# Kernel tuning notes

Hardware: AMD Instinct MI355X
Metric: run time of the kernel (lower is better)

## Reference

```python
import jax, jax.numpy as jnp
import numpy as np

N, F, RBF, E = 25000, 64, 32, 400000
RC = 5.0  # maximum_interaction_radius


def _tensor_norm(t):
    # Frobenius norm squared over the trailing 3x3 dims
    return (t ** 2).sum((-2, -1))


def _decompose(t):
    # X = I + A + S (irreducible decomposition of 3x3 blocks)
    diag_mean = jnp.trace(t, axis1=-2, axis2=-1) / 3.0
    I = diag_mean[..., None, None] * jnp.eye(3, dtype=t.dtype)
    A = 0.5 * (t - jnp.swapaxes(t, -2, -1))
    S = 0.5 * (t + jnp.swapaxes(t, -2, -1)) - I
    return I, A, S


def _lin(t, W):
    # feature-dim linear (no bias) on [N, F, 3, 3]
    return jnp.einsum('nfij,gf->ngij', t, W)


def setup_inputs():
    key = jax.random.key(0)
    ks = jax.random.split(key, 17)
    f32 = jnp.float32
    return {
        'X': jax.random.normal(ks[0], (N, F, 3, 3), f32),
        'pair_indices': jax.random.randint(ks[1], (2, E), 0, N),
        'd_ij': jax.random.uniform(ks[2], (E, 1), f32) * RC,
        'radial_feature_vector': jax.random.normal(ks[3], (E, RBF), f32),
        'atomic_charges': jax.random.normal(ks[4], (N,), f32) * 0.1,
        'W1': jax.random.normal(ks[5], (F, RBF), f32) / np.sqrt(RBF),
        'b1': jnp.zeros((F,), f32),
        'W2': jax.random.normal(ks[6], (2 * F, F), f32) / np.sqrt(F),
        'b2': jnp.zeros((2 * F,), f32),
        'W3': jax.random.normal(ks[7], (3 * F, 2 * F), f32) / np.sqrt(2 * F),
        'b3': jnp.zeros((3 * F,), f32),
        'Wl0': jax.random.normal(ks[8], (F, F), f32) / np.sqrt(F),
        'Wl1': jax.random.normal(ks[9], (F, F), f32) / np.sqrt(F),
        'Wl2': jax.random.normal(ks[10], (F, F), f32) / np.sqrt(F),
        'Wl3': jax.random.normal(ks[11], (F, F), f32) / np.sqrt(F),
        'Wl4': jax.random.normal(ks[12], (F, F), f32) / np.sqrt(F),
        'Wl5': jax.random.normal(ks[13], (F, F), f32) / np.sqrt(F),
    }


def reference(X, pair_indices, d_ij, radial_feature_vector, atomic_charges,
              W1, b1, W2, b2, W3, b3, Wl0, Wl1, Wl2, Wl3, Wl4, Wl5):
    act = jax.nn.silu
    # cosine attenuation cutoff
    C = jnp.where(d_ij < RC, 0.5 * (jnp.cos(jnp.pi * d_ij / RC) + 1.0), 0.0).reshape(-1, 1)
    # mlp_scalar: rbf -> F -> 2F -> 3F, SiLU after each Dense
    h = act(radial_feature_vector @ W1.T + b1)
    h = act(h @ W2.T + b2)
    h = act(h @ W3.T + b3) * C
    rfv = h.reshape(-1, F, 3)  # [E, F, 3]

    Xn = X / (_tensor_norm(X) + 1.0)[..., None, None]
    I, A, S = _decompose(Xn)
    I = _lin(I, Wl0)
    A = _lin(A, Wl1)
    S = _lin(S, Wl2)
    Y = I + A + S

    src, dst = pair_indices[0], pair_indices[1]

    def mp(comp, t):
        # gather-scale-scatter: [E,F,1,1] * gather([N,F,3,3]) -> scatter-add
        msg = comp[:, :, None, None] * t[dst]
        return jax.ops.segment_sum(msg, src, num_segments=N)

    msg = mp(rfv[..., 0], I) + mp(rfv[..., 1], A) + mp(rfv[..., 2], S)

    # O(3) branch
    MA = jnp.matmul(msg, Y)
    MB = jnp.matmul(Y, msg)
    scale = 1.0 + 0.1 * atomic_charges[:, None, None, None]
    I, A, S = _decompose(scale * (MA + MB))
    normp1 = (_tensor_norm(I + A + S) + 1.0)[..., None, None]
    I, A, S = I / normp1, A / normp1, S / normp1
    I = _lin(I, Wl3)
    A = _lin(A, Wl4)
    S = _lin(S, Wl5)
    dX = I + A + S
    return Xn + dX + scale * jnp.matmul(dX, dX)
```

## Files before the change

### kernel.cpp

```cpp
#include <hip/hip_runtime.h>
#include <hip/hip_fp16.h>
#include <math.h>

#ifndef M_PI
#define M_PI 3.14159265358979323846
#endif


typedef _Float16 f16x8 __attribute__((ext_vector_type(8)));
typedef float f32x4 __attribute__((ext_vector_type(4)));

#define AROW 216
#define MLPFRAGS 34816
#define WLFRAG 4096

__device__ __forceinline__ float silu_f(float x) {
    return x / (1.0f + __expf(-x));
}

__device__ __forceinline__ void recon(const float u[9], float M[9]) {
    M[0] =  u[0] + u[4];
    M[1] =  u[1] + u[5];
    M[2] =  u[2] + u[6];
    M[3] = -u[1] + u[5];
    M[4] =  u[0] + u[7];
    M[5] =  u[3] + u[8];
    M[6] = -u[2] + u[6];
    M[7] = -u[3] + u[8];
    M[8] =  u[0] - u[4] - u[7];
}

__global__ __launch_bounds__(256) void k_wcvt(
    const float* __restrict__ W1, const float* __restrict__ W2,
    const float* __restrict__ W3,
    const float* __restrict__ Wl0, const float* __restrict__ Wl1,
    const float* __restrict__ Wl2, const float* __restrict__ Wl3,
    const float* __restrict__ Wl4, const float* __restrict__ Wl5,
    __half* __restrict__ Wf)
{
    int idx = blockIdx.x * 256 + threadIdx.x;
    if (idx >= MLPFRAGS + 6 * WLFRAG) return;
    float v;
    if (idx < MLPFRAGS) {
        int frag = idx >> 9;
        int r = idx & 511;
        int l = r >> 3, j = r & 7;
        int l15 = l & 15, lg = l >> 4;
        if (frag < 4) {
            int ct = frag;
            v = W1[(ct * 16 + l15) * 32 + (lg * 8 + j)];
        } else if (frag < 20) {
            int f2 = frag - 4;
            int ct = f2 >> 1, ks = f2 & 1;
            v = W2[(ct * 16 + l15) * 64 + (ks * 32 + lg * 8 + j)];
        } else {
            int f3 = frag - 20;
            int ct = f3 >> 2, ks = f3 & 3;
            v = W3[(ct * 16 + l15) * 128 + (ks * 32 + lg * 8 + j)];
        }
    } else {
        int r2 = idx - MLPFRAGS;
        int wIdx = r2 >> 12;
        int rr = r2 & 4095;
        int f = rr >> 9;
        int ct = f >> 1, ks = f & 1;
        int elem = rr & 511;
        int l = elem >> 3, j = elem & 7;
        int l15 = l & 15, lg = l >> 4;
        const float* W = (wIdx == 0) ? Wl0 : (wIdx == 1) ? Wl1 : (wIdx == 2) ? Wl2
                       : (wIdx == 3) ? Wl3 : (wIdx == 4) ? Wl4 : Wl5;
        v = W[(ct * 16 + l15) * 64 + (ks * 32 + lg * 8 + j)];
    }
    Wf[idx] = __float2half(v);
}

__global__ __launch_bounds__(256) void k_head(
    const float* __restrict__ X, const __half* __restrict__ Wfrag,
    __half2* __restrict__ TgP, uint2* __restrict__ Tg456, int N)
{
    __shared__ __half u2l[9 * 32 * 72];
    __shared__ float s_x[2304];
    int tid = threadIdx.x;
    int n0 = blockIdx.x * 32;
    size_t total = (size_t)N * 576;

    for (int ch = 0; ch < 8; ++ch) {
        size_t base = (size_t)(n0 + ch * 4) * 576;
        for (int idx = tid; idx < 2304; idx += 256) {
            size_t gi = base + idx;
            s_x[idx] = (gi < total) ? X[gi] : 0.f;
        }
        __syncthreads();
        int w = tid >> 6, f = tid & 63;
        int node = ch * 4 + w;
        float m[9]; float n2 = 0.f;
#pragma unroll
        for (int i = 0; i < 9; ++i) { m[i] = s_x[w * 576 + f * 9 + i]; n2 += m[i] * m[i]; }
        float inv = 1.0f / (n2 + 1.0f);
#pragma unroll
        for (int i = 0; i < 9; ++i) m[i] *= inv;
        float lam = (m[0] + m[4] + m[8]) * (1.f / 3.f);
        u2l[(0 * 32 + node) * 72 + f] = __float2half(lam);
        u2l[(1 * 32 + node) * 72 + f] = __float2half(0.5f * (m[1] - m[3]));
        u2l[(2 * 32 + node) * 72 + f] = __float2half(0.5f * (m[2] - m[6]));
        u2l[(3 * 32 + node) * 72 + f] = __float2half(0.5f * (m[5] - m[7]));
        u2l[(4 * 32 + node) * 72 + f] = __float2half(m[0] - lam);
        u2l[(5 * 32 + node) * 72 + f] = __float2half(0.5f * (m[1] + m[3]));
        u2l[(6 * 32 + node) * 72 + f] = __float2half(0.5f * (m[2] + m[6]));
        u2l[(7 * 32 + node) * 72 + f] = __float2half(m[4] - lam);
        u2l[(8 * 32 + node) * 72 + f] = __float2half(0.5f * (m[5] + m[7]));
        __syncthreads();
    }

    int w = tid >> 6, lane = tid & 63;
    int l15 = lane & 15, lg = lane >> 4;
    const f32x4 z = {0.f, 0.f, 0.f, 0.f};
    f32x4 acc[5][4];
#pragma unroll
    for (int q = 0; q < 5; ++q) {
        int cm = w + q * 4;
        if (cm < 18) {
            int c = cm >> 1, rt = cm & 1;
            int gsel = (c == 0) ? 0 : (c < 4 ? 1 : 2);
            const f16x8* WFc = (const f16x8*)(Wfrag + gsel * WLFRAG);
            int abase = (c * 32 + rt * 16 + l15) * 72;
            f16x8 a0 = *(const f16x8*)&u2l[abase + lg * 8];
            f16x8 a1 = *(const f16x8*)&u2l[abase + 32 + lg * 8];
#pragma unroll
            for (int ct = 0; ct < 4; ++ct) {
                acc[q][ct] = __builtin_amdgcn_mfma_f32_16x16x32_f16(a0, WFc[(ct * 2 + 0) * 64 + lane], z, 0, 0, 0);
                acc[q][ct] = __builtin_amdgcn_mfma_f32_16x16x32_f16(a1, WFc[(ct * 2 + 1) * 64 + lane], acc[q][ct], 0, 0, 0);
            }
        }
    }
    __syncthreads();
#pragma unroll
    for (int q = 0; q < 5; ++q) {
        int cm = w + q * 4;
        if (cm < 18) {
            int c = cm >> 1, rt = cm & 1;
#pragma unroll
            for (int ct = 0; ct < 4; ++ct)
#pragma unroll
                for (int r = 0; r < 4; ++r)
                    u2l[(c * 32 + rt * 16 + lg * 4 + r) * 72 + ct * 16 + l15] =
                        __float2half(acc[q][ct][r]);
        }
    }
    __syncthreads();

    size_t slab = (size_t)N * 64;
    for (int e = 0; e < 8; ++e) {
        int idx = e * 256 + tid;
        int node = idx >> 6;
        int n = n0 + node;
        if (n >= N) continue;
        int f = idx & 63;
        size_t t = (size_t)n * 64 + f;
        const int pa[3] = {0, 2, 7};
#pragma unroll
        for (int pr = 0; pr < 3; ++pr) {
            __half a = u2l[(pa[pr] * 32 + node) * 72 + f];
            __half b = u2l[((pa[pr] + 1) * 32 + node) * 72 + f];
            TgP[(size_t)pr * slab + t] = __halves2half2(a, b);
        }
        __half2 lo = __halves2half2(u2l[(4 * 32 + node) * 72 + f],
                                    u2l[(5 * 32 + node) * 72 + f]);
        __half2 hi = __halves2half2(u2l[(6 * 32 + node) * 72 + f], __float2half(0.f));
        uint2 pk;
        pk.x = *(unsigned int*)&lo;
        pk.y = *(unsigned int*)&hi;
        Tg456[t] = pk;
    }
}

__global__ __launch_bounds__(256) void k_hist(
    const int* __restrict__ pair, int* __restrict__ count, int E)
{
    int e = blockIdx.x * 256 + threadIdx.x;
    if (e < E) atomicAdd(&count[pair[e]], 1);
}

__global__ __launch_bounds__(1024) void k_scan(
    const int* __restrict__ count, int* __restrict__ off,
    int* __restrict__ cursor, int N, int E)
{
    __shared__ int s[1024];
    __shared__ int s_carry;
    int tid = threadIdx.x;
    if (tid == 0) s_carry = 0;
    __syncthreads();
    const int CH = 32;
    for (int base = 0; base < N; base += 1024 * CH) {
        int b0 = base + tid * CH;
        int local[CH]; int sum = 0;
#pragma unroll
        for (int i = 0; i < CH; ++i) {
            int idx = b0 + i;
            int v = (idx < N) ? count[idx] : 0;
            local[i] = sum; sum += v;
        }
        s[tid] = sum;
        __syncthreads();
        for (int d = 1; d < 1024; d <<= 1) {
            int t2 = (tid >= d) ? s[tid - d] : 0;
            __syncthreads();
            s[tid] += t2;
            __syncthreads();
        }
        int excl0 = s_carry + s[tid] - sum;
#pragma unroll
        for (int i = 0; i < CH; ++i) {
            int idx = b0 + i;
            if (idx < N) { int e = excl0 + local[i]; off[idx] = e; cursor[idx] = e; }
        }
        __syncthreads();
        if (tid == 1023) s_carry += s[1023];
        __syncthreads();
    }
    if (tid == 0) off[N] = E;
}

__global__ __launch_bounds__(256) void k_scatter_sort(
    const int* __restrict__ pair, int* __restrict__ cursor,
    int* __restrict__ eOf, int* __restrict__ dstp, int* __restrict__ srcp, int E)
{
    int e = blockIdx.x * 256 + threadIdx.x;
    if (e < E) {
        int s = pair[e];
        int d = pair[(size_t)E + e];
        int pos = atomicAdd(&cursor[s], 1);
        eOf[pos] = e;
        dstp[pos] = d;
        srcp[pos] = s;
    }
}

__global__ __launch_bounds__(256) void k_edge_sorted(
    const float* __restrict__ radial, const float* __restrict__ d_ij,
    const int* __restrict__ eOf, const int* __restrict__ dstp,
    const int* __restrict__ srcp,
    const __half* __restrict__ Wf,
    const float* __restrict__ b1, const float* __restrict__ b2,
    const float* __restrict__ b3,
    const __half2* __restrict__ TgP, const uint2* __restrict__ Tg456,
    float* __restrict__ msg, int E, int N)
{
    __shared__ __half s_act[64 * AROW];
    __shared__ float s_C[64];
    __shared__ int s_e[64];
    __shared__ int s_src[64];
    __shared__ int s_dst[64];
    int tid = threadIdx.x;
    int p0 = blockIdx.x * 64;

    if (tid < 64) {
        int p = p0 + tid;
        int e = -1, s = 0, d = 0; float C = 0.f;
        if (p < E) {
            e = eOf[p];
            s = srcp[p];
            d = dstp[p];
            float dd = d_ij[e];
            C = (dd < 5.0f) ? 0.5f * (cosf((float)M_PI * dd * 0.2f) + 1.0f) : 0.0f;
        }
        s_e[tid] = e; s_src[tid] = s; s_dst[tid] = d * 64; s_C[tid] = C;
    }
    __syncthreads();

    {
        int j = tid >> 2;
        int kk = (tid & 3) * 8;
        int e = s_e[j];
        float4 v0 = make_float4(0.f, 0.f, 0.f, 0.f), v1 = v0;
        if (e >= 0) {
            v0 = *(const float4*)(radial + (size_t)e * 32 + kk);
            v1 = *(const float4*)(radial + (size_t)e * 32 + kk + 4);
        }
        __half2* dst = (__half2*)&s_act[j * AROW + kk];
        dst[0] = __floats2half2_rn(v0.x, v0.y);
        dst[1] = __floats2half2_rn(v0.z, v0.w);
        dst[2] = __floats2half2_rn(v1.x, v1.y);
        dst[3] = __floats2half2_rn(v1.z, v1.w);
    }
    __syncthreads();

    int w = tid >> 6;
    int lane = tid & 63;
    int l15 = lane & 15, lg = lane >> 4;
    const int row0 = w * 16;
    const int arow = (row0 + l15) * AROW;
    const int orow = (row0 + lg * 4) * AROW;
    const f16x8* WF = (const f16x8*)Wf;
    const f32x4 zacc = {0.f, 0.f, 0.f, 0.f};

    {
        f16x8 a = *(const f16x8*)&s_act[arow + lg * 8];
        f32x4 acc[4];
#pragma unroll
        for (int ct = 0; ct < 4; ++ct)
            acc[ct] = __builtin_amdgcn_mfma_f32_16x16x32_f16(a, WF[ct * 64 + lane], zacc, 0, 0, 0);
        __syncthreads();
#pragma unroll
        for (int ct = 0; ct < 4; ++ct) {
            int o = ct * 16 + l15;
            float bias = b1[o];
#pragma unroll
            for (int r = 0; r < 4; ++r)
                s_act[orow + r * AROW + o] = __float2half(silu_f(acc[ct][r] + bias));
        }
        __syncthreads();
    }

    {
        f16x8 a0 = *(const f16x8*)&s_act[arow + 0 * 32 + lg * 8];
        f16x8 a1 = *(const f16x8*)&s_act[arow + 1 * 32 + lg * 8];
        f32x4 acc[8];
#pragma unroll
        for (int ct = 0; ct < 8; ++ct) {
            acc[ct] = __builtin_amdgcn_mfma_f32_16x16x32_f16(a0, WF[(4 + ct * 2 + 0) * 64 + lane], zacc, 0, 0, 0);
            acc[ct] = __builtin_amdgcn_mfma_f32_16x16x32_f16(a1, WF[(4 + ct * 2 + 1) * 64 + lane], acc[ct], 0, 0, 0);
        }
        __syncthreads();
#pragma unroll
        for (int ct = 0; ct < 8; ++ct) {
            int o = ct * 16 + l15;
            float bias = b2[o];
#pragma unroll
            for (int r = 0; r < 4; ++r)
                s_act[orow + r * AROW + o] = __float2half(silu_f(acc[ct][r] + bias));
        }
        __syncthreads();
    }

    {
        f16x8 a[4];
#pragma unroll
        for (int ks = 0; ks < 4; ++ks)
            a[ks] = *(const f16x8*)&s_act[arow + ks * 32 + lg * 8];
        float Cr[4];
#pragma unroll
        for (int r = 0; r < 4; ++r) Cr[r] = s_C[row0 + lg * 4 + r];
        __syncthreads();
#pragma unroll
        for (int ct = 0; ct < 12; ++ct) {
            f32x4 acc = zacc;
#pragma unroll
            for (int ks = 0; ks < 4; ++ks)
                acc = __builtin_amdgcn_mfma_f32_16x16x32_f16(a[ks], WF[(20 + ct * 4 + ks) * 64 + lane], acc, 0, 0, 0);
            int o = ct * 16 + l15;
            float bias = b3[o];
            int f = o / 3;
            int cmp = o - f * 3;
            int col = cmp * 64 + f;
#pragma unroll
            for (int r = 0; r < 4; ++r)
                s_act[orow + r * AROW + col] = __float2half(silu_f(acc[r] + bias) * Cr[r]);
        }
        __syncthreads();
    }

    {
        int wv = __builtin_amdgcn_readfirstlane(w);
        size_t slab = (size_t)N * 64;
        int jmax = min(64, E - p0);

        if (wv == 2) {
            const uint2* T4 = Tg456;
            auto flush3 = [&](int cur, int gs, int ge, float a0, float a1, float a2) {
                bool lb = (gs == 0) || (srcp[gs - 1] != cur);
                bool rb = (ge >= E) || (srcp[ge] != cur);
                size_t b = (size_t)cur * 64 + lane;
                if (lb && rb) {
                    msg[4 * slab + b] = a0;
                    msg[5 * slab + b] = a1;
                    msg[6 * slab + b] = a2;
                } else {
                    atomicAdd(&msg[4 * slab + b], a0);
                    atomicAdd(&msg[5 * slab + b], a1);
                    atomicAdd(&msg[6 * slab + b], a2);
                }
            };
            float A00 = 0.f, A01 = 0.f, A02 = 0.f, A10 = 0.f, A11 = 0.f, A12 = 0.f;
            float A20 = 0.f, A21 = 0.f, A22 = 0.f, A30 = 0.f, A31 = 0.f, A32 = 0.f;
            int cur0 = -1, cur1 = -1, cur2 = -1, cur3 = -1;
            int js0 = 0, js1 = 0, js2 = 0, js3 = 0;
            uint2 tv0 = make_uint2(0, 0), tv1 = tv0, tv2 = tv0, tv3 = tv0;
            if (0 < jmax)  tv0 = T4[(size_t)s_dst[0]  + lane];
            if (16 < jmax) tv1 = T4[(size_t)s_dst[16] + lane];
            if (32 < jmax) tv2 = T4[(size_t)s_dst[32] + lane];
            if (48 < jmax) tv3 = T4[(size_t)s_dst[48] + lane];
#define MS3(BASE, CUR, JS, A0, A1, A2, TV) { \
            int j = (BASE) + t; \
            if (j < jmax) { \
                uint2 tvc = TV; \
                int jn = j + 1; \
                if (jn < (BASE) + 16 && jn < jmax) \
                    TV = T4[(size_t)s_dst[jn] + lane]; \
                int s = __builtin_amdgcn_readfirstlane(s_src[j]); \
                if (s != CUR) { if (CUR >= 0) flush3(CUR, p0 + JS, p0 + j, A0, A1, A2); \
                                CUR = s; JS = j; A0 = 0.f; A1 = 0.f; A2 = 0.f; } \
                float rf = __half2float(s_act[j * AROW + 128 + lane]); \
                float2 lof = __half22float2(*(__half2*)&tvc.x); \
                __half2 hic = *(__half2*)&tvc.y; \
                A0 += rf * lof.x; A1 += rf * lof.y; \
                A2 += rf * __half2float(hic.x); \
            } }
            for (int t = 0; t < 16; ++t) {
                MS3(0,  cur0, js0, A00, A01, A02, tv0)
                MS3(16, cur1, js1, A10, A11, A12, tv1)
                MS3(32, cur2, js2, A20, A21, A22, tv2)
                MS3(48, cur3, js3, A30, A31, A32, tv3)
            }
#undef MS3
            if (cur0 >= 0) flush3(cur0, p0 + js0, p0 + min(16, jmax), A00, A01, A02);
            if (cur1 >= 0) flush3(cur1, p0 + js1, p0 + min(32, jmax), A10, A11, A12);
            if (cur2 >= 0) flush3(cur2, p0 + js2, p0 + min(48, jmax), A20, A21, A22);
            if (cur3 >= 0) flush3(cur3, p0 + js3, p0 + min(64, jmax), A30, A31, A32);
        } else {
            int pr = (wv == 3) ? 2 : wv;
            int c0 = (wv == 0) ? 0 : ((wv == 1) ? 2 : 7);
            int c1 = c0 + 1;
            int offA = (wv == 0) ? lane : ((wv == 1) ? (64 + lane) : (128 + lane));
            int offB = 64 + lane;
            bool W0 = (wv == 0);
            const unsigned int* TP = (const unsigned int*)TgP + (size_t)pr * slab;
            auto flush2 = [&](int cur, int gs, int ge, float a0, float a1) {
                bool lb = (gs == 0) || (srcp[gs - 1] != cur);
                bool rb = (ge >= E) || (srcp[ge] != cur);
                size_t b = (size_t)cur * 64 + lane;
                if (lb && rb) {
                    msg[(size_t)c0 * slab + b] = a0;
                    msg[(size_t)c1 * slab + b] = a1;
                } else {
                    atomicAdd(&msg[(size_t)c0 * slab + b], a0);
                    atomicAdd(&msg[(size_t)c1 * slab + b], a1);
                }
            };
            float A00 = 0.f, A01 = 0.f, A10 = 0.f, A11 = 0.f;
            float A20 = 0.f, A21 = 0.f, A30 = 0.f, A31 = 0.f;
            int cur0 = -1, cur1 = -1, cur2 = -1, cur3 = -1;
            int js0 = 0, js1 = 0, js2 = 0, js3 = 0;
            unsigned int tv0 = 0, tv1 = 0, tv2 = 0, tv3 = 0;
            if (0 < jmax)  tv0 = TP[(size_t)s_dst[0]  + lane];
            if (16 < jmax) tv1 = TP[(size_t)s_dst[16] + lane];
            if (32 < jmax) tv2 = TP[(size_t)s_dst[32] + lane];
            if (48 < jmax) tv3 = TP[(size_t)s_dst[48] + lane];
#define MS2(BASE, CUR, JS, A0, A1, TV) { \
            int j = (BASE) + t; \
            if (j < jmax) { \
                unsigned int tvc = TV; \
                int jn = j + 1; \
                if (jn < (BASE) + 16 && jn < jmax) \
                    TV = TP[(size_t)s_dst[jn] + lane]; \
                int s = __builtin_amdgcn_readfirstlane(s_src[j]); \
                if (s != CUR) { if (CUR >= 0) flush2(CUR, p0 + JS, p0 + j, A0, A1); \
                                CUR = s; JS = j; A0 = 0.f; A1 = 0.f; } \
                float2 tvf = __half22float2(*(__half2*)&tvc); \
                float rfA = __half2float(s_act[j * AROW + offA]); \
                float rfB = W0 ? __half2float(s_act[j * AROW + offB]) : rfA; \
                A0 += rfA * tvf.x; A1 += rfB * tvf.y; \
            } }
            for (int t = 0; t < 16; ++t) {
                MS2(0,  cur0, js0, A00, A01, tv0)
                MS2(16, cur1, js1, A10, A11, tv1)
                MS2(32, cur2, js2, A20, A21, tv2)
                MS2(48, cur3, js3, A30, A31, tv3)
            }
#undef MS2
            if (cur0 >= 0) flush2(cur0, p0 + js0, p0 + min(16, jmax), A00, A01);
            if (cur1 >= 0) flush2(cur1, p0 + js1, p0 + min(32, jmax), A10, A11);
            if (cur2 >= 0) flush2(cur2, p0 + js2, p0 + min(48, jmax), A20, A21);
            if (cur3 >= 0) flush2(cur3, p0 + js3, p0 + min(64, jmax), A30, A31);
        }
    }
}

__global__ __launch_bounds__(256) void k_tail(
    const float* __restrict__ msg,
    const __half2* __restrict__ TgP, const uint2* __restrict__ Tg456,
    const float* __restrict__ X, const float* __restrict__ charges,
    const __half* __restrict__ Wfrag, float* __restrict__ out, int N)
{
    __shared__ __half u2l[9 * 32 * 72];
    __shared__ float s_sc[32];
    int tid = threadIdx.x;
    int n0 = blockIdx.x * 32;
    size_t slab = (size_t)N * 64;

    if (tid < 32) {
        int n = n0 + tid;
        s_sc[tid] = (n < N) ? 1.0f + 0.1f * charges[n] : 0.f;
    }
    __syncthreads();

    for (int e = 0; e < 8; ++e) {
        int idx = e * 256 + tid;
        int node = idx >> 6;
        int n = n0 + node;
        float um[9], uy[9];
        if (n < N) {
            size_t t = (size_t)n0 * 64 + idx;
#pragma unroll
            for (int c = 0; c < 9; ++c)
                um[c] = msg[(size_t)c * slab + t];
            float2 p0 = __half22float2(TgP[0 * slab + t]);
            float2 p1 = __half22float2(TgP[1 * slab + t]);
            float2 p2 = __half22float2(TgP[2 * slab + t]);
            uint2 q = Tg456[t];
            float2 q0 = __half22float2(*(__half2*)&q.x);
            __half2 q1 = *(__half2*)&q.y;
            uy[0] = p0.x; uy[1] = p0.y;
            uy[2] = p1.x; uy[3] = p1.y;
            uy[4] = q0.x; uy[5] = q0.y;
            uy[6] = __half2float(q1.x);
            uy[7] = p2.x; uy[8] = p2.y;
        } else {
#pragma unroll
            for (int c = 0; c < 9; ++c) { um[c] = 0.f; uy[c] = 0.f; }
        }
        float M[9], Y[9];
        recon(um, M);
        recon(uy, Y);
        float P[9];
#pragma unroll
        for (int i = 0; i < 3; ++i)
#pragma unroll
            for (int j = 0; j < 3; ++j) {
                float s = 0.f;
#pragma unroll
                for (int k = 0; k < 3; ++k)
                    s += M[i * 3 + k] * Y[k * 3 + j] + Y[i * 3 + k] * M[k * 3 + j];
                P[i * 3 + j] = s;
            }
        float sc = s_sc[node];
        float nrm = 0.f;
#pragma unroll
        for (int i = 0; i < 9; ++i) { P[i] *= sc; nrm += P[i] * P[i]; }
        float inv = 1.0f / (nrm + 1.0f);
        float lam = (P[0] + P[4] + P[8]) * (1.f / 3.f);
        int f = idx & 63;
        u2l[(0 * 32 + node) * 72 + f] = __float2half(lam * inv);
        u2l[(1 * 32 + node) * 72 + f] = __float2half(0.5f * (P[1] - P[3]) * inv);
        u2l[(2 * 32 + node) * 72 + f] = __float2half(0.5f * (P[2] - P[6]) * inv);
        u2l[(3 * 32 + node) * 72 + f] = __float2half(0.5f * (P[5] - P[7]) * inv);
        u2l[(4 * 32 + node) * 72 + f] = __float2half((P[0] - lam) * inv);
        u2l[(5 * 32 + node) * 72 + f] = __float2half(0.5f * (P[1] + P[3]) * inv);
        u2l[(6 * 32 + node) * 72 + f] = __float2half(0.5f * (P[2] + P[6]) * inv);
        u2l[(7 * 32 + node) * 72 + f] = __float2half((P[4] - lam) * inv);
        u2l[(8 * 32 + node) * 72 + f] = __float2half(0.5f * (P[5] + P[7]) * inv);
    }
    __syncthreads();

    int w = tid >> 6, lane = tid & 63;
    int l15 = lane & 15, lg = lane >> 4;
    const f32x4 z = {0.f, 0.f, 0.f, 0.f};
    f32x4 acc[5][4];
#pragma unroll
    for (int q = 0; q < 5; ++q) {
        int cm = w + q * 4;
        if (cm < 18) {
            int c = cm >> 1, rt = cm & 1;
            int gsel = (c == 0) ? 0 : (c < 4 ? 1 : 2);
            const f16x8* WFc = (const f16x8*)(Wfrag + gsel * WLFRAG);
            int abase = (c * 32 + rt * 16 + l15) * 72;
            f16x8 a0 = *(const f16x8*)&u2l[abase + lg * 8];
            f16x8 a1 = *(const f16x8*)&u2l[abase + 32 + lg * 8];
#pragma unroll
            for (int ct = 0; ct < 4; ++ct) {
                acc[q][ct] = __builtin_amdgcn_mfma_f32_16x16x32_f16(a0, WFc[(ct * 2 + 0) * 64 + lane], z, 0, 0, 0);
                acc[q][ct] = __builtin_amdgcn_mfma_f32_16x16x32_f16(a1, WFc[(ct * 2 + 1) * 64 + lane], acc[q][ct], 0, 0, 0);
            }
        }
    }
    __syncthreads();
#pragma unroll
    for (int q = 0; q < 5; ++q) {
        int cm = w + q * 4;
        if (cm < 18) {
            int c = cm >> 1, rt = cm & 1;
#pragma unroll
            for (int ct = 0; ct < 4; ++ct)
#pragma unroll
                for (int r = 0; r < 4; ++r)
                    u2l[(c * 32 + rt * 16 + lg * 4 + r) * 72 + ct * 16 + l15] =
                        __float2half(acc[q][ct][r]);
        }
    }
    __syncthreads();

    for (int e = 0; e < 8; ++e) {
        int idx = e * 256 + tid;
        int node = idx >> 6;
        int n = n0 + node;
        if (n >= N) continue;
        int f = idx & 63;
        float v[9];
#pragma unroll
        for (int c = 0; c < 9; ++c)
            v[c] = __half2float(u2l[(c * 32 + node) * 72 + f]);
        float dX[9];
        recon(v, dX);
        const float* xp = X + (size_t)n * 576 + f * 9;
        float m[9]; float n2 = 0.f;
#pragma unroll
        for (int i = 0; i < 9; ++i) { m[i] = xp[i]; n2 += m[i] * m[i]; }
        float invn = 1.0f / (n2 + 1.0f);
#pragma unroll
        for (int i = 0; i < 9; ++i) m[i] *= invn;
        float sc = s_sc[node];
        float* op = out + (size_t)n * 576 + f * 9;
#pragma unroll
        for (int i = 0; i < 3; ++i)
#pragma unroll
            for (int j = 0; j < 3; ++j) {
                float s = 0.f;
#pragma unroll
                for (int k = 0; k < 3; ++k) s += dX[i * 3 + k] * dX[k * 3 + j];
                op[i * 3 + j] = m[i * 3 + j] + dX[i * 3 + j] + sc * s;
            }
    }
}

extern "C" void kernel_launch(void* const* d_in, const int* in_sizes, int n_in,
                              void* d_out, int out_size, void* d_ws, size_t ws_size,
                              hipStream_t stream)
{
    const float* X       = (const float*)d_in[0];
    const int*   pair    = (const int*)d_in[1];
    const float* dij     = (const float*)d_in[2];
    const float* radial  = (const float*)d_in[3];
    const float* charges = (const float*)d_in[4];
    const float* W1  = (const float*)d_in[5];
    const float* b1  = (const float*)d_in[6];
    const float* W2  = (const float*)d_in[7];
    const float* b2  = (const float*)d_in[8];
    const float* W3  = (const float*)d_in[9];
    const float* b3  = (const float*)d_in[10];
    const float* Wl0 = (const float*)d_in[11];
    const float* Wl1 = (const float*)d_in[12];
    const float* Wl2 = (const float*)d_in[13];
    const float* Wl3 = (const float*)d_in[14];
    const float* Wl4 = (const float*)d_in[15];
    const float* Wl5 = (const float*)d_in[16];

    int N = in_sizes[4];
    int E = in_sizes[2];
    int nb_edge = (E + 63) / 64;
    int nb_node32 = (N + 31) / 32;
    size_t slab = (size_t)N * 64;
    size_t slab9 = slab * 9;

    float* B = (float*)d_ws;
    __half2* TgP = (__half2*)(B + slab9);
    uint2* Tg456 = (uint2*)((__half*)TgP + 6 * slab);
    __half* Wf  = (__half*)(Tg456 + slab);
    int* ints   = (int*)(Wf + MLPFRAGS + 6 * WLFRAG);
    int* count  = ints;
    int* off    = count + N;
    int* cursor = off + N + 1;
    int* eOf    = cursor + N;
    int* dstp   = eOf + E;
    int* srcp   = dstp + E;

    hipMemsetAsync(count, 0, (size_t)N * sizeof(int), stream);
    hipMemsetAsync(B, 0, slab9 * sizeof(float), stream);

    int nWf = MLPFRAGS + 6 * WLFRAG;
    k_wcvt<<<(nWf + 255) / 256, 256, 0, stream>>>(W1, W2, W3,
                                                  Wl0, Wl1, Wl2, Wl3, Wl4, Wl5, Wf);
    k_head<<<nb_node32, 256, 0, stream>>>(X, Wf + MLPFRAGS, TgP, Tg456, N);

    k_hist<<<(E + 255) / 256, 256, 0, stream>>>(pair, count, E);
    k_scan<<<1, 1024, 0, stream>>>(count, off, cursor, N, E);
    k_scatter_sort<<<(E + 255) / 256, 256, 0, stream>>>(pair, cursor, eOf, dstp, srcp, E);

    k_edge_sorted<<<nb_edge, 256, 0, stream>>>(radial, dij, eOf, dstp, srcp,
                                               Wf, b1, b2, b3, TgP, Tg456, B, E, N);

    k_tail<<<nb_node32, 256, 0, stream>>>(B, TgP, Tg456, X, charges,
                                          Wf + MLPFRAGS + 3 * WLFRAG,
                                          (float*)d_out, N);
}
```

Measured before the change: 414.5 us.

## Accumulate messages in packed fp16, pack sorted edge records, deepen gather prefetch

Message accumulation moves from nine fp32 slabs to five packed-half2 slabs. Flushes become half2 stores or global_atomic_pk_add_f16, which roughly halves scatter traffic, atomic count, the memset and the tail read. The sort kernel now writes one uint4 record per edge holding src, dst*64, edge id and the precomputed cutoff C, replacing three separate int arrays and the d_ij gather in the edge kernel. The gather prefetch in the message loops is deepened from one to two edges ahead. Accumulating atomically in fp16 reduces precision and could exceed tolerance for high-degree nodes.

```diff
diff --git a/kernel.cpp b/kernel.cpp
--- a/kernel.cpp
+++ b/kernel.cpp
@@ -16,6 +16,11 @@
 
 __device__ __forceinline__ float silu_f(float x) {
     return x / (1.0f + __expf(-x));
+}
+
+__device__ __forceinline__ void pk_add_f16(__half2* addr, __half2 val) {
+    asm volatile("global_atomic_pk_add_f16 %0, %1, off"
+                 :: "v"(addr), "v"(val) : "memory");
 }
 
 __device__ __forceinline__ void recon(const float u[9], float M[9]) {
@@ -222,29 +227,32 @@
 }
 
 __global__ __launch_bounds__(256) void k_scatter_sort(
-    const int* __restrict__ pair, int* __restrict__ cursor,
-    int* __restrict__ eOf, int* __restrict__ dstp, int* __restrict__ srcp, int E)
+    const int* __restrict__ pair, const float* __restrict__ d_ij,
+    int* __restrict__ cursor, uint4* __restrict__ esd, int E)
 {
     int e = blockIdx.x * 256 + threadIdx.x;
     if (e < E) {
         int s = pair[e];
         int d = pair[(size_t)E + e];
+        float dd = d_ij[e];
+        float C = (dd < 5.0f) ? 0.5f * (cosf((float)M_PI * dd * 0.2f) + 1.0f) : 0.0f;
         int pos = atomicAdd(&cursor[s], 1);
-        eOf[pos] = e;
-        dstp[pos] = d;
-        srcp[pos] = s;
+        uint4 v;
+        v.x = (unsigned int)s;
+        v.y = (unsigned int)(d * 64);
+        v.z = (unsigned int)e;
+        v.w = __float_as_uint(C);
+        esd[pos] = v;
     }
 }
 
 __global__ __launch_bounds__(256) void k_edge_sorted(
-    const float* __restrict__ radial, const float* __restrict__ d_ij,
-    const int* __restrict__ eOf, const int* __restrict__ dstp,
-    const int* __restrict__ srcp,
+    const float* __restrict__ radial, const uint4* __restrict__ esd,
     const __half* __restrict__ Wf,
     const float* __restrict__ b1, const float* __restrict__ b2,
     const float* __restrict__ b3,
     const __half2* __restrict__ TgP, const uint2* __restrict__ Tg456,
-    float* __restrict__ msg, int E, int N)
+    __half2* __restrict__ msgP, int E, int N)
 {
     __shared__ __half s_act[64 * AROW];
     __shared__ float s_C[64];
@@ -256,15 +264,12 @@
 
     if (tid < 64) {
         int p = p0 + tid;
-        int e = -1, s = 0, d = 0; float C = 0.f;
+        int e = -1, s = 0, d64 = 0; float C = 0.f;
         if (p < E) {
-            e = eOf[p];
-            s = srcp[p];
-            d = dstp[p];
-            float dd = d_ij[e];
-            C = (dd < 5.0f) ? 0.5f * (cosf((float)M_PI * dd * 0.2f) + 1.0f) : 0.0f;
-        }
-        s_e[tid] = e; s_src[tid] = s; s_dst[tid] = d * 64; s_C[tid] = C;
+            uint4 v = esd[p];
+            s = (int)v.x; d64 = (int)v.y; e = (int)v.z; C = __uint_as_float(v.w);
+        }
+        s_e[tid] = e; s_src[tid] = s; s_dst[tid] = d64; s_C[tid] = C;
     }
     __syncthreads();
 
@@ -368,35 +373,40 @@
         if (wv == 2) {
             const uint2* T4 = Tg456;
             auto flush3 = [&](int cur, int gs, int ge, float a0, float a1, float a2) {
-                bool lb = (gs == 0) || (srcp[gs - 1] != cur);
-                bool rb = (ge >= E) || (srcp[ge] != cur);
+                bool lb = (gs == 0) || ((int)esd[gs - 1].x != cur);
+                bool rb = (ge >= E) || ((int)esd[ge].x != cur);
                 size_t b = (size_t)cur * 64 + lane;
+                __half2 h45 = __floats2half2_rn(a0, a1);
+                __half2 h6  = __floats2half2_rn(a2, 0.f);
                 if (lb && rb) {
-                    msg[4 * slab + b] = a0;
-                    msg[5 * slab + b] = a1;
-                    msg[6 * slab + b] = a2;
+                    msgP[3 * slab + b] = h45;
+                    msgP[4 * slab + b] = h6;
                 } else {
-                    atomicAdd(&msg[4 * slab + b], a0);
-                    atomicAdd(&msg[5 * slab + b], a1);
-                    atomicAdd(&msg[6 * slab + b], a2);
+                    pk_add_f16(&msgP[3 * slab + b], h45);
+                    pk_add_f16(&msgP[4 * slab + b], h6);
                 }
             };
             float A00 = 0.f, A01 = 0.f, A02 = 0.f, A10 = 0.f, A11 = 0.f, A12 = 0.f;
             float A20 = 0.f, A21 = 0.f, A22 = 0.f, A30 = 0.f, A31 = 0.f, A32 = 0.f;
             int cur0 = -1, cur1 = -1, cur2 = -1, cur3 = -1;
             int js0 = 0, js1 = 0, js2 = 0, js3 = 0;
-            uint2 tv0 = make_uint2(0, 0), tv1 = tv0, tv2 = tv0, tv3 = tv0;
-            if (0 < jmax)  tv0 = T4[(size_t)s_dst[0]  + lane];
-            if (16 < jmax) tv1 = T4[(size_t)s_dst[16] + lane];
-            if (32 < jmax) tv2 = T4[(size_t)s_dst[32] + lane];
-            if (48 < jmax) tv3 = T4[(size_t)s_dst[48] + lane];
-#define MS3(BASE, CUR, JS, A0, A1, A2, TV) { \
+            uint2 ta0 = make_uint2(0, 0), ta1 = ta0, ta2 = ta0, ta3 = ta0;
+            uint2 tb0 = ta0, tb1 = ta0, tb2 = ta0, tb3 = ta0;
+            if (0 < jmax)  ta0 = T4[(size_t)s_dst[0]  + lane];
+            if (16 < jmax) ta1 = T4[(size_t)s_dst[16] + lane];
+            if (32 < jmax) ta2 = T4[(size_t)s_dst[32] + lane];
+            if (48 < jmax) ta3 = T4[(size_t)s_dst[48] + lane];
+            if (1 < jmax)  tb0 = T4[(size_t)s_dst[1]  + lane];
+            if (17 < jmax) tb1 = T4[(size_t)s_dst[17] + lane];
+            if (33 < jmax) tb2 = T4[(size_t)s_dst[33] + lane];
+            if (49 < jmax) tb3 = T4[(size_t)s_dst[49] + lane];
+#define MS3(BASE, CUR, JS, A0, A1, A2, TVA, TVB) { \
             int j = (BASE) + t; \
             if (j < jmax) { \
-                uint2 tvc = TV; \
-                int jn = j + 1; \
+                uint2 tvc = TVA; TVA = TVB; \
+                int jn = j + 2; \
                 if (jn < (BASE) + 16 && jn < jmax) \
-                    TV = T4[(size_t)s_dst[jn] + lane]; \
+                    TVB = T4[(size_t)s_dst[jn] + lane]; \
                 int s = __builtin_amdgcn_readfirstlane(s_src[j]); \
                 if (s != CUR) { if (CUR >= 0) flush3(CUR, p0 + JS, p0 + j, A0, A1, A2); \
                                 CUR = s; JS = j; A0 = 0.f; A1 = 0.f; A2 = 0.f; } \
@@ -407,10 +417,10 @@
                 A2 += rf * __half2float(hic.x); \
             } }
             for (int t = 0; t < 16; ++t) {
-                MS3(0,  cur0, js0, A00, A01, A02, tv0)
-                MS3(16, cur1, js1, A10, A11, A12, tv1)
-                MS3(32, cur2, js2, A20, A21, A22, tv2)
-                MS3(48, cur3, js3, A30, A31, A32, tv3)
+                MS3(0,  cur0, js0, A00, A01, A02, ta0, tb0)
+                MS3(16, cur1, js1, A10, A11, A12, ta1, tb1)
+                MS3(32, cur2, js2, A20, A21, A22, ta2, tb2)
+                MS3(48, cur3, js3, A30, A31, A32, ta3, tb3)
             }
 #undef MS3
             if (cur0 >= 0) flush3(cur0, p0 + js0, p0 + min(16, jmax), A00, A01, A02);
@@ -418,41 +428,43 @@
             if (cur2 >= 0) flush3(cur2, p0 + js2, p0 + min(48, jmax), A20, A21, A22);
             if (cur3 >= 0) flush3(cur3, p0 + js3, p0 + min(64, jmax), A30, A31, A32);
         } else {
-            int pr = (wv == 3) ? 2 : wv;
-            int c0 = (wv == 0) ? 0 : ((wv == 1) ? 2 : 7);
-            int c1 = c0 + 1;
+            int sl = (wv == 0) ? 0 : ((wv == 1) ? 1 : 2);
             int offA = (wv == 0) ? lane : ((wv == 1) ? (64 + lane) : (128 + lane));
             int offB = 64 + lane;
             bool W0 = (wv == 0);
-            const unsigned int* TP = (const unsigned int*)TgP + (size_t)pr * slab;
+            const unsigned int* TP = (const unsigned int*)TgP + (size_t)sl * slab;
             auto flush2 = [&](int cur, int gs, int ge, float a0, float a1) {
-                bool lb = (gs == 0) || (srcp[gs - 1] != cur);
-                bool rb = (ge >= E) || (srcp[ge] != cur);
+                bool lb = (gs == 0) || ((int)esd[gs - 1].x != cur);
+                bool rb = (ge >= E) || ((int)esd[ge].x != cur);
                 size_t b = (size_t)cur * 64 + lane;
+                __half2 hv = __floats2half2_rn(a0, a1);
                 if (lb && rb) {
-                    msg[(size_t)c0 * slab + b] = a0;
-                    msg[(size_t)c1 * slab + b] = a1;
+                    msgP[(size_t)sl * slab + b] = hv;
                 } else {
-                    atomicAdd(&msg[(size_t)c0 * slab + b], a0);
-                    atomicAdd(&msg[(size_t)c1 * slab + b], a1);
+                    pk_add_f16(&msgP[(size_t)sl * slab + b], hv);
                 }
             };
             float A00 = 0.f, A01 = 0.f, A10 = 0.f, A11 = 0.f;
             float A20 = 0.f, A21 = 0.f, A30 = 0.f, A31 = 0.f;
             int cur0 = -1, cur1 = -1, cur2 = -1, cur3 = -1;
             int js0 = 0, js1 = 0, js2 = 0, js3 = 0;
-            unsigned int tv0 = 0, tv1 = 0, tv2 = 0, tv3 = 0;
-            if (0 < jmax)  tv0 = TP[(size_t)s_dst[0]  + lane];
-            if (16 < jmax) tv1 = TP[(size_t)s_dst[16] + lane];
-            if (32 < jmax) tv2 = TP[(size_t)s_dst[32] + lane];
-            if (48 < jmax) tv3 = TP[(size_t)s_dst[48] + lane];
-#define MS2(BASE, CUR, JS, A0, A1, TV) { \
+            unsigned int ta0 = 0, ta1 = 0, ta2 = 0, ta3 = 0;
+            unsigned int tb0 = 0, tb1 = 0, tb2 = 0, tb3 = 0;
+            if (0 < jmax)  ta0 = TP[(size_t)s_dst[0]  + lane];
+            if (16 < jmax) ta1 = TP[(size_t)s_dst[16] + lane];
+            if (32 < jmax) ta2 = TP[(size_t)s_dst[32] + lane];
+            if (48 < jmax) ta3 = TP[(size_t)s_dst[48] + lane];
+            if (1 < jmax)  tb0 = TP[(size_t)s_dst[1]  + lane];
+            if (17 < jmax) tb1 = TP[(size_t)s_dst[17] + lane];
+            if (33 < jmax) tb2 = TP[(size_t)s_dst[33] + lane];
+            if (49 < jmax) tb3 = TP[(size_t)s_dst[49] + lane];
+#define MS2(BASE, CUR, JS, A0, A1, TVA, TVB) { \
             int j = (BASE) + t; \
             if (j < jmax) { \
-                unsigned int tvc = TV; \
-                int jn = j + 1; \
+                unsigned int tvc = TVA; TVA = TVB; \
+                int jn = j + 2; \
                 if (jn < (BASE) + 16 && jn < jmax) \
-                    TV = TP[(size_t)s_dst[jn] + lane]; \
+                    TVB = TP[(size_t)s_dst[jn] + lane]; \
                 int s = __builtin_amdgcn_readfirstlane(s_src[j]); \
                 if (s != CUR) { if (CUR >= 0) flush2(CUR, p0 + JS, p0 + j, A0, A1); \
                                 CUR = s; JS = j; A0 = 0.f; A1 = 0.f; } \
@@ -462,10 +474,10 @@
                 A0 += rfA * tvf.x; A1 += rfB * tvf.y; \
             } }
             for (int t = 0; t < 16; ++t) {
-                MS2(0,  cur0, js0, A00, A01, tv0)
-                MS2(16, cur1, js1, A10, A11, tv1)
-                MS2(32, cur2, js2, A20, A21, tv2)
-                MS2(48, cur3, js3, A30, A31, tv3)
+                MS2(0,  cur0, js0, A00, A01, ta0, tb0)
+                MS2(16, cur1, js1, A10, A11, ta1, tb1)
+                MS2(32, cur2, js2, A20, A21, ta2, tb2)
+                MS2(48, cur3, js3, A30, A31, ta3, tb3)
             }
 #undef MS2
             if (cur0 >= 0) flush2(cur0, p0 + js0, p0 + min(16, jmax), A00, A01);
@@ -477,7 +489,7 @@
 }
 
 __global__ __launch_bounds__(256) void k_tail(
-    const float* __restrict__ msg,
+    const __half2* __restrict__ msgP,
     const __half2* __restrict__ TgP, const uint2* __restrict__ Tg456,
     const float* __restrict__ X, const float* __restrict__ charges,
     const __half* __restrict__ Wfrag, float* __restrict__ out, int N)
@@ -501,9 +513,16 @@
         float um[9], uy[9];
         if (n < N) {
             size_t t = (size_t)n0 * 64 + idx;
-#pragma unroll
-            for (int c = 0; c < 9; ++c)
-                um[c] = msg[(size_t)c * slab + t];
+            float2 m01 = __half22float2(msgP[0 * slab + t]);
+            float2 m23 = __half22float2(msgP[1 * slab + t]);
+            float2 m78 = __half22float2(msgP[2 * slab + t]);
+            float2 m45 = __half22float2(msgP[3 * slab + t]);
+            float2 m6_ = __half22float2(msgP[4 * slab + t]);
+            um[0] = m01.x; um[1] = m01.y;
+            um[2] = m23.x; um[3] = m23.y;
+            um[4] = m45.x; um[5] = m45.y;
+            um[6] = m6_.x;
+            um[7] = m78.x; um[8] = m78.y;
             float2 p0 = __half22float2(TgP[0 * slab + t]);
             float2 p1 = __half22float2(TgP[1 * slab + t]);
             float2 p2 = __half22float2(TgP[2 * slab + t]);
@@ -649,22 +668,19 @@
     int nb_edge = (E + 63) / 64;
     int nb_node32 = (N + 31) / 32;
     size_t slab = (size_t)N * 64;
-    size_t slab9 = slab * 9;
-
-    float* B = (float*)d_ws;
-    __half2* TgP = (__half2*)(B + slab9);
-    uint2* Tg456 = (uint2*)((__half*)TgP + 6 * slab);
-    __half* Wf  = (__half*)(Tg456 + slab);
-    int* ints   = (int*)(Wf + MLPFRAGS + 6 * WLFRAG);
+
+    __half2* msgP = (__half2*)d_ws;
+    __half2* TgP  = msgP + 5 * slab;
+    uint2* Tg456  = (uint2*)(TgP + 3 * slab);
+    __half* Wf    = (__half*)(Tg456 + slab);
+    uint4* esd    = (uint4*)(Wf + MLPFRAGS + 6 * WLFRAG);
+    int* ints   = (int*)(esd + E);
     int* count  = ints;
     int* off    = count + N;
     int* cursor = off + N + 1;
-    int* eOf    = cursor + N;
-    int* dstp   = eOf + E;
-    int* srcp   = dstp + E;
 
     hipMemsetAsync(count, 0, (size_t)N * sizeof(int), stream);
-    hipMemsetAsync(B, 0, slab9 * sizeof(float), stream);
+    hipMemsetAsync(msgP, 0, 5 * slab * sizeof(__half2), stream);
 
     int nWf = MLPFRAGS + 6 * WLFRAG;
     k_wcvt<<<(nWf + 255) / 256, 256, 0, stream>>>(W1, W2, W3,
@@ -673,12 +689,13 @@
 
     k_hist<<<(E + 255) / 256, 256, 0, stream>>>(pair, count, E);
     k_scan<<<1, 1024, 0, stream>>>(count, off, cursor, N, E);
-    k_scatter_sort<<<(E + 255) / 256, 256, 0, stream>>>(pair, cursor, eOf, dstp, srcp, E);
-
-    k_edge_sorted<<<nb_edge, 256, 0, stream>>>(radial, dij, eOf, dstp, srcp,
-                                               Wf, b1, b2, b3, TgP, Tg456, B, E, N);
-
-    k_tail<<<nb_node32, 256, 0, stream>>>(B, TgP, Tg456, X, charges,
+    k_scatter_sort<<<(E + 255) / 256, 256, 0, stream>>>(pair, dij, cursor, esd, E);
+
+    k_edge_sorted<<<nb_edge, 256, 0, stream>>>(radial, esd,
+                                               Wf, b1, b2, b3, TgP, Tg456,
+                                               msgP, E, N);
+
+    k_tail<<<nb_node32, 256, 0, stream>>>(msgP, TgP, Tg456, X, charges,
                                           Wf + MLPFRAGS + 3 * WLFRAG,
                                           (float*)d_out, N);
 }
```

Result: faster. 395.4 us (-4.6%).
